# Kernel tuning notes

Measured on AMD Instinct MI355X. Metric: run time of the kernel, lower is better.

Reference implementation:

```python
import jax, jax.numpy as jnp
import numpy as np

NUM_HEADS = 8
MODEL_DIM = 1024
SEQ_LEN = 2048


def setup_inputs() -> dict:
    key = jax.random.key(0)
    ks = jax.random.split(key, 9)
    H, D, L = NUM_HEADS, MODEL_DIM, SEQ_LEN
    s_in = 1.0 / np.sqrt(D)
    s_out = 1.0 / np.sqrt(H * D)
    return {
        "tokens": jax.random.normal(ks[0], (D, L), dtype=jnp.float32),
        "Wq": jax.random.uniform(ks[1], (H * D, D), jnp.float32, -s_in, s_in),
        "bq": jax.random.uniform(ks[2], (H * D,), jnp.float32, -s_in, s_in),
        "Wk": jax.random.uniform(ks[3], (H * D, D), jnp.float32, -s_in, s_in),
        "bk": jax.random.uniform(ks[4], (H * D,), jnp.float32, -s_in, s_in),
        "Wv": jax.random.uniform(ks[5], (H * D, D), jnp.float32, -s_in, s_in),
        "bv": jax.random.uniform(ks[6], (H * D,), jnp.float32, -s_in, s_in),
        "Wo": jax.random.uniform(ks[7], (D, H * D), jnp.float32, -s_out, s_out),
        "bo": jax.random.uniform(ks[8], (D,), jnp.float32, -s_out, s_out),
    }


def _split_heads(x, H, D, L):
    # Faithful to torch: raw .view of contiguous [H*D, L] into (L, H, D),
    # then permute(1, 2, 0) -> (H, D, L). This is a memory reinterpretation,
    # not a transpose, exactly as in the original module.
    return x.reshape(L, H, D).transpose(1, 2, 0)


def reference(tokens, Wq, bq, Wk, bk, Wv, bv, Wo, bo):
    D, L = tokens.shape
    H = Wq.shape[0] // D
    # 1x1 Conv1d == matmul over channel dim
    q = _split_heads(Wq @ tokens + bq[:, None], H, D, L)  # (H, D, L)
    k = _split_heads(Wk @ tokens + bk[:, None], H, D, L)  # (H, D, L)
    v = _split_heads(Wv @ tokens + bv[:, None], H, D, L)  # (H, D, L)
    scores = jnp.einsum("hdl,hdm->hlm", q, k) / np.sqrt(D)  # (H, L, L)
    # torch F.softmax without dim on a 3D tensor -> dim=0 (head axis)
    attn = jax.nn.softmax(scores, axis=0)
    ctx = jnp.einsum("hlm,hdm->hdl", attn, v)  # (H, D, L)
    out = Wo @ ctx.reshape(H * D, L) + bo[:, None]  # (D, L)
    return out
```

## Files before the change

### kernel.cpp

```cpp
#include <hip/hip_runtime.h>

#define SEQL 2048
#define DMODEL 1024
#define HDIM 8192

typedef unsigned short bf16_t;
typedef __attribute__((ext_vector_type(8))) short bf16x8;
typedef __attribute__((ext_vector_type(4))) float f32x4;

__device__ __forceinline__ bf16_t f2bf(float f) {
  unsigned u = __float_as_uint(f);
  u += 0x7fffu + ((u >> 16) & 1u);
  return (bf16_t)(u >> 16);
}
__device__ __forceinline__ float bf2f(bf16_t b) {
  return __uint_as_float(((unsigned)b) << 16);
}

__global__ __launch_bounds__(256) void cvt_f32_bf16(const float* __restrict__ in,
                                                    bf16_t* __restrict__ out, int n) {
  int i = (blockIdx.x * 256 + threadIdx.x) * 4;
  if (i >= n) return;
  float4 f = *reinterpret_cast<const float4*>(in + i);
  ushort4 u;
  u.x = f2bf(f.x); u.y = f2bf(f.y); u.z = f2bf(f.z); u.w = f2bf(f.w);
  *reinterpret_cast<ushort4*>(out + i) = u;
}

__global__ __launch_bounds__(256) void cvt3_f32_bf16(const float* __restrict__ a,
                                                     const float* __restrict__ b,
                                                     const float* __restrict__ c,
                                                     bf16_t* __restrict__ out) {
  const int SEG = HDIM * DMODEL;
  int i = (blockIdx.x * 256 + threadIdx.x) * 4;
  const float* src;
  int off;
  if (i < SEG) { src = a; off = i; }
  else if (i < 2 * SEG) { src = b; off = i - SEG; }
  else { src = c; off = i - 2 * SEG; }
  float4 f = *reinterpret_cast<const float4*>(src + off);
  ushort4 u;
  u.x = f2bf(f.x); u.y = f2bf(f.y); u.z = f2bf(f.z); u.w = f2bf(f.w);
  *reinterpret_cast<ushort4*>(out + i) = u;
}

__global__ __launch_bounds__(256) void bias3(const float* __restrict__ a,
                                             const float* __restrict__ b,
                                             const float* __restrict__ c,
                                             float* __restrict__ out) {
  int i = blockIdx.x * 256 + threadIdx.x;
  float v = (i < HDIM) ? a[i] : (i < 2 * HDIM) ? b[i - HDIM] : c[i - 2 * HDIM];
  out[i] = v;
}

__global__ __launch_bounds__(256) void transpose_cvt(const float* __restrict__ in,
                                                     bf16_t* __restrict__ out) {
  __shared__ float tile[32][33];
  int bx = blockIdx.x * 32;
  int by = blockIdx.y * 32;
  int tx = threadIdx.x, ty = threadIdx.y;
#pragma unroll
  for (int i = ty; i < 32; i += 8)
    tile[i][tx] = in[(size_t)(by + i) * SEQL + bx + tx];
  __syncthreads();
#pragma unroll
  for (int i = ty; i < 32; i += 8)
    out[(size_t)(bx + i) * DMODEL + by + tx] = f2bf(tile[tx][i]);
}

__global__ __launch_bounds__(256) void softmax_heads(bf16_t* __restrict__ S) {
  const size_t HS = (size_t)SEQL * SEQL;
  size_t p = ((size_t)blockIdx.x * 256 + threadIdx.x) * 8;
  float v[8][8];
#pragma unroll
  for (int h = 0; h < 8; ++h) {
    bf16x8 x = *reinterpret_cast<const bf16x8*>(S + h * HS + p);
#pragma unroll
    for (int e = 0; e < 8; ++e) v[h][e] = bf2f((bf16_t)x[e]);
  }
#pragma unroll
  for (int e = 0; e < 8; ++e) {
    float mx = v[0][e];
#pragma unroll
    for (int h = 1; h < 8; ++h) mx = fmaxf(mx, v[h][e]);
    float s = 0.f;
#pragma unroll
    for (int h = 0; h < 8; ++h) { v[h][e] = __expf(v[h][e] - mx); s += v[h][e]; }
    float inv = 1.0f / s;
#pragma unroll
    for (int h = 0; h < 8; ++h) v[h][e] *= inv;
  }
#pragma unroll
  for (int h = 0; h < 8; ++h) {
    bf16x8 x;
#pragma unroll
    for (int e = 0; e < 8; ++e) x[e] = (short)f2bf(v[h][e]);
    *reinterpret_cast<bf16x8*>(S + h * HS + p) = x;
  }
}

__global__ __launch_bounds__(256) void reduce_out(const bf16_t* __restrict__ P,
                                                  const float* __restrict__ bo,
                                                  float* __restrict__ out) {
  const size_t NEL = (size_t)DMODEL * SEQL;
  size_t i = ((size_t)blockIdx.x * 256 + threadIdx.x) * 8;
  float s[8] = {0.f, 0.f, 0.f, 0.f, 0.f, 0.f, 0.f, 0.f};
#pragma unroll
  for (int z = 0; z < 8; ++z) {
    bf16x8 x = *reinterpret_cast<const bf16x8*>(P + z * NEL + i);
#pragma unroll
    for (int e = 0; e < 8; ++e) s[e] += bf2f((bf16_t)x[e]);
  }
  float bias = bo[i >> 11];
  float4 o0 = {s[0] + bias, s[1] + bias, s[2] + bias, s[3] + bias};
  float4 o1 = {s[4] + bias, s[5] + bias, s[6] + bias, s[7] + bias};
  *reinterpret_cast<float4*>(out + i) = o0;
  *reinterpret_cast<float4*>(out + i + 4) = o1;
}

template <int EPI, bool HAS_BIAS>
__global__ __launch_bounds__(512, 2) void gemm256(
    const bf16_t* __restrict__ A, const bf16_t* __restrict__ B,
    bf16_t* __restrict__ C, bf16_t* __restrict__ C2, const float* __restrict__ bias,
    int K, int lda, int ldb, int ldc,
    long long sA, long long sB, long long sC, float scale, int gx, int gxy) {
  __shared__ alignas(16) char smem[147456];
  auto* As = reinterpret_cast<bf16_t(*)[2][8192]>(smem);
  auto* Bs = reinterpret_cast<bf16_t(*)[2][8192]>(smem + 65536);
  const int nwg = gridDim.x;
  const int bid = blockIdx.x;
  const int swz = (nwg & 7) ? bid : ((bid & 7) * (nwg >> 3) + (bid >> 3));
  const int zz = swz / gxy;
  const int rem = swz - zz * gxy;
  const int brow = (rem / gx) * 256;
  const int bcol = (rem % gx) * 256;
  A += (long long)zz * sA;
  B += (long long)zz * sB;
  C += (long long)zz * sC;
  const int tid = threadIdx.x;
  const int w = tid >> 6, lane = tid & 63;
  const int fr = lane & 15, fq = lane >> 4;
  const int wr = w >> 2, wc = w & 3;

  int rj[2], cj[2];
#pragma unroll
  for (int j = 0; j < 2; ++j) {
    const int c = (w * 2 + j) * 64 + lane;
    rj[j] = c >> 3;
    cj[j] = ((c & 7) ^ (rj[j] & 7)) << 3;
  }

  auto stageA = [&](int buf, int half, int kk) {
#pragma unroll
    for (int j = 0; j < 2; ++j) {
      const bf16_t* g = A + (size_t)(brow + half * 128 + rj[j]) * lda + kk + cj[j];
      __builtin_amdgcn_global_load_lds(
          (const __attribute__((address_space(1))) void*)g,
          (__attribute__((address_space(3))) void*)(&As[buf][half][(w * 2 + j) * 512]),
          16, 0, 0);
    }
  };
  auto stageB = [&](int buf, int half, int kk) {
#pragma unroll
    for (int j = 0; j < 2; ++j) {
      const bf16_t* g = B + (size_t)(bcol + half * 128 + rj[j]) * ldb + kk + cj[j];
      __builtin_amdgcn_global_load_lds(
          (const __attribute__((address_space(1))) void*)g,
          (__attribute__((address_space(3))) void*)(&Bs[buf][half][(w * 2 + j) * 512]),
          16, 0, 0);
    }
  };

  auto ldA = [&](int buf, int mf, int kk) -> bf16x8 {
    const int rr = mf * 16 + fr;
    return *reinterpret_cast<const bf16x8*>(
        &As[buf][wr][rr * 64 + ((((kk << 2) | fq) ^ (rr & 7)) << 3)]);
  };
  auto ldB = [&](int buf, int nf, int kk) -> bf16x8 {
    const int rr = (wc & 1) * 64 + nf * 16 + fr;
    return *reinterpret_cast<const bf16x8*>(
        &Bs[buf][wc >> 1][rr * 64 + ((((kk << 2) | fq) ^ (rr & 7)) << 3)]);
  };

  f32x4 acc[8][4];
  const f32x4 fzero = {0.f, 0.f, 0.f, 0.f};
#pragma unroll
  for (int m = 0; m < 8; ++m)
#pragma unroll
    for (int n = 0; n < 4; ++n) acc[m][n] = fzero;

  const int NT = K >> 6;
  stageA(0, 0, 0); stageA(0, 1, 0); stageB(0, 0, 0); stageB(0, 1, 0);
  __syncthreads();

  for (int t = 0; t < NT; ++t) {
    const int p = t & 1, q = p ^ 1;
    const int kn = (t + 1) << 6;
    const bool pre = (t + 1 < NT);
    bf16x8 af[4][2], bg[4][2];

    if (pre) { stageA(q, 0, kn); stageA(q, 1, kn); }
#pragma unroll
    for (int mf = 0; mf < 4; ++mf)
#pragma unroll
      for (int kk = 0; kk < 2; ++kk) af[mf][kk] = ldA(p, mf, kk);
#pragma unroll
    for (int nf = 0; nf < 2; ++nf)
#pragma unroll
      for (int kk = 0; kk < 2; ++kk) bg[nf][kk] = ldB(p, nf, kk);
    __builtin_amdgcn_s_setprio(1);
#pragma unroll
    for (int mf = 0; mf < 4; ++mf)
#pragma unroll
      for (int nf = 0; nf < 2; ++nf)
#pragma unroll
        for (int kk = 0; kk < 2; ++kk)
          acc[mf][nf] = __builtin_amdgcn_mfma_f32_16x16x32_bf16(
              af[mf][kk], bg[nf][kk], acc[mf][nf], 0, 0, 0);
    __builtin_amdgcn_s_setprio(0);

    if (pre) { stageB(q, 0, kn); stageB(q, 1, kn); }
#pragma unroll
    for (int nf = 2; nf < 4; ++nf)
#pragma unroll
      for (int kk = 0; kk < 2; ++kk) bg[nf][kk] = ldB(p, nf, kk);
    __builtin_amdgcn_s_setprio(1);
#pragma unroll
    for (int mf = 0; mf < 4; ++mf)
#pragma unroll
      for (int nf = 2; nf < 4; ++nf)
#pragma unroll
        for (int kk = 0; kk < 2; ++kk)
          acc[mf][nf] = __builtin_amdgcn_mfma_f32_16x16x32_bf16(
              af[mf][kk], bg[nf][kk], acc[mf][nf], 0, 0, 0);
    __builtin_amdgcn_s_setprio(0);

#pragma unroll
    for (int mf = 0; mf < 4; ++mf)
#pragma unroll
      for (int kk = 0; kk < 2; ++kk) af[mf][kk] = ldA(p, mf + 4, kk);
    __builtin_amdgcn_s_setprio(1);
#pragma unroll
    for (int mf = 0; mf < 4; ++mf)
#pragma unroll
      for (int nf = 2; nf < 4; ++nf)
#pragma unroll
        for (int kk = 0; kk < 2; ++kk)
          acc[mf + 4][nf] = __builtin_amdgcn_mfma_f32_16x16x32_bf16(
              af[mf][kk], bg[nf][kk], acc[mf + 4][nf], 0, 0, 0);
    __builtin_amdgcn_s_setprio(0);

#pragma unroll
    for (int nf = 0; nf < 2; ++nf)
#pragma unroll
      for (int kk = 0; kk < 2; ++kk) bg[nf][kk] = ldB(p, nf, kk);
    __builtin_amdgcn_s_setprio(1);
#pragma unroll
    for (int mf = 0; mf < 4; ++mf)
#pragma unroll
      for (int nf = 0; nf < 2; ++nf)
#pragma unroll
        for (int kk = 0; kk < 2; ++kk)
          acc[mf + 4][nf] = __builtin_amdgcn_mfma_f32_16x16x32_bf16(
              af[mf][kk], bg[nf][kk], acc[mf + 4][nf], 0, 0, 0);
    __builtin_amdgcn_s_setprio(0);

    if (pre) __syncthreads();
  }

  __syncthreads();

  const bool vseg = (EPI == 2) && (brow >= 2 * HDIM);
  if ((EPI == 0) || ((EPI == 2) && !vseg)) {
    bf16_t* Ct = (bf16_t*)smem;
#pragma unroll
    for (int mf = 0; mf < 8; ++mf)
#pragma unroll
      for (int j = 0; j < 4; ++j) {
        const int orow = wr * 128 + mf * 16 + fq * 4 + j;
        float bvv = HAS_BIAS ? bias[brow + orow] : 0.f;
#pragma unroll
        for (int nf = 0; nf < 4; ++nf)
          Ct[orow * 264 + wc * 64 + nf * 16 + fr] = f2bf(acc[mf][nf][j] * scale + bvv);
      }
    __syncthreads();
#pragma unroll
    for (int i = 0; i < 16; ++i) {
      const int c = tid + i * 512;
      const int row = c >> 5, ch = c & 31;
      *reinterpret_cast<bf16x8*>(&C[(size_t)(brow + row) * ldc + bcol + ch * 8]) =
          *reinterpret_cast<const bf16x8*>(smem + row * 528 + ch * 16);
    }
  } else if constexpr (EPI == 2) {
    const int vrow = brow - 2 * HDIM;
    bf16_t* Vt = (bf16_t*)smem;
#pragma unroll
    for (int mf = 0; mf < 8; ++mf)
#pragma unroll
      for (int j = 0; j < 4; ++j) {
        const int i = wr * 128 + mf * 16 + fq * 4 + j;
        const int mloc = i >> 2;
        float bvv = HAS_BIAS ? bias[brow + i] : 0.f;
#pragma unroll
        for (int nf = 0; nf < 4; ++nf) {
          const int dloc = wc * 64 + nf * 16 + fr;
          Vt[(j * 256 + dloc) * 72 + mloc] = f2bf(acc[mf][nf][j] * scale + bvv);
        }
      }
    __syncthreads();
    const int r_ = bcol >> 10, d0 = bcol & 1023, m0 = vrow >> 2;
#pragma unroll
    for (int sIt = 0; sIt < 2; ++sIt) {
      const int s = tid + sIt * 512;
      const int h2 = s >> 8, dloc = s & 255;
      const bf16_t* src = Vt + (h2 * 256 + dloc) * 72;
      bf16_t* dst = C2 + ((size_t)(2 * h2 + r_) * DMODEL + d0 + dloc) * SEQL + m0;
#pragma unroll
      for (int qq = 0; qq < 8; ++qq)
        *reinterpret_cast<bf16x8*>(dst + qq * 8) =
            *reinterpret_cast<const bf16x8*>(src + qq * 8);
    }
  }
}

extern "C" void kernel_launch(void* const* d_in, const int* in_sizes, int n_in,
                              void* d_out, int out_size, void* d_ws, size_t ws_size,
                              hipStream_t stream) {
  const float* tokens = (const float*)d_in[0];
  const float* Wq = (const float*)d_in[1];
  const float* bq = (const float*)d_in[2];
  const float* Wk = (const float*)d_in[3];
  const float* bk = (const float*)d_in[4];
  const float* Wv = (const float*)d_in[5];
  const float* bv = (const float*)d_in[6];
  const float* Wo = (const float*)d_in[7];
  const float* bo = (const float*)d_in[8];
  float* out = (float*)d_out;
  char* ws = (char*)d_ws;
  const size_t MB = 1024ull * 1024ull;
  bf16_t* Vs = (bf16_t*)(ws + 0);
  bf16_t* QmKm = (bf16_t*)(ws + 32 * MB);
  bf16_t* Qm = QmKm;
  bf16_t* Km = QmKm + (size_t)HDIM * SEQL;
  bf16_t* Sb = (bf16_t*)(ws + 96 * MB);
  bf16_t* tT = (bf16_t*)(ws + 96 * MB);
  bf16_t* Wqkv = (bf16_t*)(ws + 100 * MB);
  float* bqkv = (float*)(ws + 148 * MB);
  bf16_t* cT = (bf16_t*)(ws + 32 * MB);
  bf16_t* Wob = (bf16_t*)(ws + 64 * MB);
  bf16_t* Pp = (bf16_t*)(ws + 96 * MB);

  dim3 b256(256);
  dim3 b512(512);
  const int nW = HDIM * DMODEL;

  transpose_cvt<<<dim3(SEQL / 32, DMODEL / 32), dim3(32, 8), 0, stream>>>(tokens, tT);
  cvt3_f32_bf16<<<3 * nW / 1024, b256, 0, stream>>>(Wq, Wk, Wv, Wqkv);
  bias3<<<3 * HDIM / 256, b256, 0, stream>>>(bq, bk, bv, bqkv);

  gemm256<2, true><<<dim3(768, 1, 1), b512, 0, stream>>>(
      Wqkv, tT, QmKm, Vs, bqkv, DMODEL, DMODEL, DMODEL, SEQL,
      0, 0, 0, 1.0f, 8, 768);

  gemm256<0, false><<<dim3(512, 1, 1), b512, 0, stream>>>(
      Qm, Km, Sb, nullptr, nullptr, DMODEL, HDIM, HDIM, SEQL,
      1024, 1024, (long long)SEQL * SEQL, 0.03125f, 8, 64);

  softmax_heads<<<(SEQL * SEQL / 8) / 256, b256, 0, stream>>>(Sb);

  gemm256<0, false><<<dim3(256, 1, 1), b512, 0, stream>>>(
      Sb, Vs, cT, nullptr, nullptr, SEQL, SEQL, SEQL, HDIM,
      (long long)SEQL * SEQL, (long long)DMODEL * SEQL, 1024, 1.0f, 4, 32);

  cvt_f32_bf16<<<nW / 1024, b256, 0, stream>>>(Wo, Wob, nW);
  gemm256<0, false><<<dim3(256, 1, 1), b512, 0, stream>>>(
      Wob, cT, Pp, nullptr, nullptr, 1024, HDIM, HDIM, SEQL,
      1024, 1024, (long long)DMODEL * SEQL, 1.0f, 8, 32);
  reduce_out<<<(DMODEL * SEQL / 8) / 256, b256, 0, stream>>>(Pp, bo, out);
}
```

Measured before the change: 356.2 us.

## Triple-buffer A tiles and use partial vmcnt waits in GEMM main loop

```diff
diff --git a/kernel.cpp b/kernel.cpp
--- a/kernel.cpp
+++ b/kernel.cpp
@@ -124,9 +124,9 @@
     bf16_t* __restrict__ C, bf16_t* __restrict__ C2, const float* __restrict__ bias,
     int K, int lda, int ldb, int ldc,
     long long sA, long long sB, long long sC, float scale, int gx, int gxy) {
-  __shared__ alignas(16) char smem[147456];
+  __shared__ alignas(16) char smem[163840];
   auto* As = reinterpret_cast<bf16_t(*)[2][8192]>(smem);
-  auto* Bs = reinterpret_cast<bf16_t(*)[2][8192]>(smem + 65536);
+  auto* Bs = reinterpret_cast<bf16_t(*)[2][8192]>(smem + 98304);
   const int nwg = gridDim.x;
   const int bid = blockIdx.x;
   const int swz = (nwg & 7) ? bid : ((bid & 7) * (nwg >> 3) + (bid >> 3));
@@ -150,25 +150,29 @@
     cj[j] = ((c & 7) ^ (rj[j] & 7)) << 3;
   }
 
-  auto stageA = [&](int buf, int half, int kk) {
-#pragma unroll
-    for (int j = 0; j < 2; ++j) {
-      const bf16_t* g = A + (size_t)(brow + half * 128 + rj[j]) * lda + kk + cj[j];
-      __builtin_amdgcn_global_load_lds(
-          (const __attribute__((address_space(1))) void*)g,
-          (__attribute__((address_space(3))) void*)(&As[buf][half][(w * 2 + j) * 512]),
-          16, 0, 0);
-    }
+  auto stageA = [&](int buf, int kk) {
+#pragma unroll
+    for (int half = 0; half < 2; ++half)
+#pragma unroll
+      for (int j = 0; j < 2; ++j) {
+        const bf16_t* g = A + (size_t)(brow + half * 128 + rj[j]) * lda + kk + cj[j];
+        __builtin_amdgcn_global_load_lds(
+            (const __attribute__((address_space(1))) void*)g,
+            (__attribute__((address_space(3))) void*)(&As[buf][half][(w * 2 + j) * 512]),
+            16, 0, 0);
+      }
   };
-  auto stageB = [&](int buf, int half, int kk) {
-#pragma unroll
-    for (int j = 0; j < 2; ++j) {
-      const bf16_t* g = B + (size_t)(bcol + half * 128 + rj[j]) * ldb + kk + cj[j];
-      __builtin_amdgcn_global_load_lds(
-          (const __attribute__((address_space(1))) void*)g,
-          (__attribute__((address_space(3))) void*)(&Bs[buf][half][(w * 2 + j) * 512]),
-          16, 0, 0);
-    }
+  auto stageB = [&](int buf, int kk) {
+#pragma unroll
+    for (int half = 0; half < 2; ++half)
+#pragma unroll
+      for (int j = 0; j < 2; ++j) {
+        const bf16_t* g = B + (size_t)(bcol + half * 128 + rj[j]) * ldb + kk + cj[j];
+        __builtin_amdgcn_global_load_lds(
+            (const __attribute__((address_space(1))) void*)g,
+            (__attribute__((address_space(3))) void*)(&Bs[buf][half][(w * 2 + j) * 512]),
+            16, 0, 0);
+      }
   };
 
   auto ldA = [&](int buf, int mf, int kk) -> bf16x8 {
@@ -190,24 +194,31 @@
     for (int n = 0; n < 4; ++n) acc[m][n] = fzero;
 
   const int NT = K >> 6;
-  stageA(0, 0, 0); stageA(0, 1, 0); stageB(0, 0, 0); stageB(0, 1, 0);
-  __syncthreads();
-
+
+  stageA(0, 0);
+  stageB(0, 0);
+  stageA(1, 64);
+  asm volatile("s_waitcnt vmcnt(4)" ::: "memory");
+  __builtin_amdgcn_sched_barrier(0);
+  __builtin_amdgcn_s_barrier();
+  __builtin_amdgcn_sched_barrier(0);
+
+  int pa = 0;
   for (int t = 0; t < NT; ++t) {
-    const int p = t & 1, q = p ^ 1;
-    const int kn = (t + 1) << 6;
-    const bool pre = (t + 1 < NT);
+    const int pb = t & 1;
+    const bool pre1 = (t + 1 < NT), pre2 = (t + 2 < NT);
+    int sa = pa + 2; if (sa >= 3) sa -= 3;
     bf16x8 af[4][2], bg[4][2];
 
-    if (pre) { stageA(q, 0, kn); stageA(q, 1, kn); }
-#pragma unroll
-    for (int mf = 0; mf < 4; ++mf)
-#pragma unroll
-      for (int kk = 0; kk < 2; ++kk) af[mf][kk] = ldA(p, mf, kk);
+    if (pre1) stageB(pb ^ 1, (t + 1) << 6);
+#pragma unroll
+    for (int mf = 0; mf < 4; ++mf)
+#pragma unroll
+      for (int kk = 0; kk < 2; ++kk) af[mf][kk] = ldA(pa, mf, kk);
 #pragma unroll
     for (int nf = 0; nf < 2; ++nf)
 #pragma unroll
-      for (int kk = 0; kk < 2; ++kk) bg[nf][kk] = ldB(p, nf, kk);
+      for (int kk = 0; kk < 2; ++kk) bg[nf][kk] = ldB(pb, nf, kk);
     __builtin_amdgcn_s_setprio(1);
 #pragma unroll
     for (int mf = 0; mf < 4; ++mf)
@@ -219,11 +230,11 @@
               af[mf][kk], bg[nf][kk], acc[mf][nf], 0, 0, 0);
     __builtin_amdgcn_s_setprio(0);
 
-    if (pre) { stageB(q, 0, kn); stageB(q, 1, kn); }
+    if (pre2) stageA(sa, (t + 2) << 6);
 #pragma unroll
     for (int nf = 2; nf < 4; ++nf)
 #pragma unroll
-      for (int kk = 0; kk < 2; ++kk) bg[nf][kk] = ldB(p, nf, kk);
+      for (int kk = 0; kk < 2; ++kk) bg[nf][kk] = ldB(pb, nf, kk);
     __builtin_amdgcn_s_setprio(1);
 #pragma unroll
     for (int mf = 0; mf < 4; ++mf)
@@ -238,7 +249,7 @@
 #pragma unroll
     for (int mf = 0; mf < 4; ++mf)
 #pragma unroll
-      for (int kk = 0; kk < 2; ++kk) af[mf][kk] = ldA(p, mf + 4, kk);
+      for (int kk = 0; kk < 2; ++kk) af[mf][kk] = ldA(pa, mf + 4, kk);
     __builtin_amdgcn_s_setprio(1);
 #pragma unroll
     for (int mf = 0; mf < 4; ++mf)
@@ -253,7 +264,7 @@
 #pragma unroll
     for (int nf = 0; nf < 2; ++nf)
 #pragma unroll
-      for (int kk = 0; kk < 2; ++kk) bg[nf][kk] = ldB(p, nf, kk);
+      for (int kk = 0; kk < 2; ++kk) bg[nf][kk] = ldB(pb, nf, kk);
     __builtin_amdgcn_s_setprio(1);
 #pragma unroll
     for (int mf = 0; mf < 4; ++mf)
@@ -265,7 +276,18 @@
               af[mf][kk], bg[nf][kk], acc[mf + 4][nf], 0, 0, 0);
     __builtin_amdgcn_s_setprio(0);
 
-    if (pre) __syncthreads();
+    if (pre1) {
+      __builtin_amdgcn_sched_barrier(0);
+      if (pre2) {
+        asm volatile("s_waitcnt vmcnt(4)" ::: "memory");
+      } else {
+        asm volatile("s_waitcnt vmcnt(0)" ::: "memory");
+      }
+      __builtin_amdgcn_sched_barrier(0);
+      __builtin_amdgcn_s_barrier();
+      __builtin_amdgcn_sched_barrier(0);
+    }
+    ++pa; if (pa >= 3) pa = 0;
   }
 
   __syncthreads();
```

After: 357.9 us. Within noise of the previous version (+0.5%).
